# Kernel optimization log

Hardware: AMD Instinct MI355X
Metric: run time of the kernel (lower is better)

The kernel has to match this reference:

```python
import jax, jax.numpy as jnp
import numpy as np

C, H, W = 32, 64, 64
KH, KW = 5, 5
OH, OW = 60, 60
N_IN = C * H * W
B, S = 64, 4096
CAP = 128


def _build_indices():
    # Enumerate every (c, kh, kw, oh, ow) slot of the unfold, matching
    # fold(unfold(order)) in the torch module (stride 1, pad 0, dilation 1).
    c = np.arange(C)[:, None, None, None, None]
    kh = np.arange(KH)[None, :, None, None, None]
    kw = np.arange(KW)[None, None, :, None, None]
    oh = np.arange(OH)[None, None, None, :, None]
    ow = np.arange(OW)[None, None, None, None, :]
    ids = c * (H * W) + (oh + kh) * W + (ow + kw)          # input flat id feeding slot
    ckk = c * (KH * KW) + kh * KW + kw                     # kernel-local channel index
    j = ckk * (OH * OW) + oh * OW + ow                     # flat slot in order_convoled
    ids, j = np.broadcast_arrays(ids, j)
    ids = ids.ravel().astype(np.int64)
    j = j.ravel().astype(np.int64)
    perm = np.argsort(ids, kind='stable')
    sid, sj = ids[perm], j[perm]
    counts = np.bincount(ids, minlength=N_IN)
    Lmax = int(counts.max())                               # = 25 here
    starts = np.concatenate([[0], np.cumsum(counts)[:-1]])
    rank = np.arange(sid.shape[0]) - starts[sid]
    indices = np.full((N_IN, Lmax), -1, dtype=np.int32)
    indices[sid, rank] = sj
    return indices


def setup_inputs() -> dict:
    key = jax.random.key(0)
    spikes = jax.random.randint(key, (B, S, 1, 1), 0, N_IN, dtype=jnp.int32)
    indices = jnp.asarray(_build_indices())
    return {"spikes": spikes, "indices": indices, "out_h": OH, "out_w": OW, "cap": CAP}


def reference(spikes, indices, out_h, out_w, cap):
    Bn, Sn = spikes.shape[0], spikes.shape[1]
    L = indices.shape[1]
    nbins = out_h * out_w
    E = Sn * L                                             # events per batch element

    ids = spikes[:, :, 0, 0]                               # [B,S] flat input ids
    g = indices[ids]                                       # [B,S,L] slots, -1 padded
    valid = g >= 0
    j = jnp.where(valid, g, 0)
    bins = (j % nbins).reshape(Bn * E)                     # output bin (oh*out_w+ow)
    ckk = (j // nbins).reshape(Bn * E)                     # kernel-local index to store
    valid_f = valid.reshape(Bn * E)
    b_idx = jnp.repeat(jnp.arange(Bn, dtype=jnp.int32), E)

    # Arrival-order rank within each (batch, bin): stable sort by global bin,
    # then rank = position - segment start (running max of change points).
    gbin = jnp.where(valid_f, b_idx * nbins + bins, Bn * nbins)   # sentinel for invalid
    perm = jnp.argsort(gbin)                               # stable
    sorted_gbin = gbin[perm]
    pos = jnp.arange(Bn * E, dtype=jnp.int32)
    change = jnp.concatenate([jnp.ones((1,), bool), sorted_gbin[1:] != sorted_gbin[:-1]])
    seg_start = jax.lax.cummax(jnp.where(change, pos, 0))
    rank_sorted = pos - seg_start
    rank = jnp.zeros(Bn * E, jnp.int32).at[perm].set(rank_sorted)  # inverse perm

    # Scatter ckk into per-bin slots; invalid / overflow events go to slot=cap (dropped).
    slot = jnp.where(valid_f & (rank < cap), rank, cap)
    out = jnp.full((Bn, cap + 1, nbins), -1, dtype=spikes.dtype)
    out = out.at[b_idx, slot, bins].set(jnp.where(valid_f, ckk, -1), mode='drop')
    return out[:, :cap].reshape(Bn, cap, out_h, out_w)
```

## Files before the change

kernel.cpp:

```cpp
#include <hip/hip_runtime.h>

#define OHh   60
#define OWw   60
#define NBINS (OHh * OWw)
#define NB    64
#define NS    4096
#define CAP   128

#define NW     4
#define SEG    (NS / NW)
#define CH     (SEG / 64)
#define HCAP   160
#define PRE0   64

__global__ __launch_bounds__(256) void sort_spikes_row4(
    const int* __restrict__ spikes, int* __restrict__ out) {
    const int bid  = (int)blockIdx.x;
    const int b    = bid & (NB - 1);
    const int row  = bid >> 6;
    const int tid  = (int)threadIdx.x;
    const int wv   = tid >> 6;
    const int lane = tid & 63;
    const bool valid = lane < OWw;

    __shared__ int            hitbuf[NW][256];
    __shared__ unsigned       pres[NW][64][7];
    __shared__ unsigned short outimg[PRE0][OWw];
    __shared__ int            cnt[NW][64];
    __shared__ int            ovf;

    if (tid == 0) ovf = 0;
#pragma unroll
    for (int i = 0; i < 5; ++i) pres[wv][lane][i] = 0u;

    {
        int* oi = (int*)&outimg[0][0];
        for (int i = tid; i < PRE0 * OWw / 2; i += 256) oi[i] = -1;
    }

    const int* __restrict__ sp   = spikes + b * NS + wv * SEG;
    int* __restrict__       outb = out + (size_t)b * (CAP * NBINS) + row * OWw;

    int vs[CH];
#pragma unroll
    for (int c = 0; c < CH; ++c) vs[c] = sp[c * 64 + lane];

    int* const hb_w = &hitbuf[wv][0];
    const int row5 = row * 5;

    int hbase = 0;
#pragma unroll
    for (int c = 0; c < CH; ++c) {
        const int v = vs[c];
        const int h = (v >> 6) & 63;
        const int w = v & 63;
        const int A = (v >> 12) * 25 + h * 5 + w - row5;
        const int R = (w << 16) | A;
        const bool halo = (unsigned)(h - row) < 5u;

        const unsigned long long mask = __ballot(halo);
        const int pos = __builtin_amdgcn_mbcnt_hi(
            (unsigned)(mask >> 32),
            __builtin_amdgcn_mbcnt_lo((unsigned)mask, 0));
        if (halo) hb_w[min(hbase + pos, 255)] = R;
        hbase += (int)__popcll(mask);

        if (valid) outb[(PRE0 + wv * CH + c) * NBINS + lane] = -1;
    }
    if (hbase > HCAP && lane == 0) ovf = 1;
    const int n = min(hbase, HCAP);

    const int qi  = (lane < OWw) ? (lane / 5) : 4096;
    const int kwc = lane - qi * 5;
    for (int hbi = 0; hbi < n; hbi += 12) {
        const int hidx = hbi + qi;
        const int R    = hb_w[min(hidx, 255)];
        const int bin  = (R >> 16) - kwc;
        if (((unsigned)bin < 60u) && (hidx < n)) {
            atomicOr(&pres[wv][bin][hidx >> 5], 1u << (hidx & 31));
        }
    }

    unsigned m0 = pres[wv][lane][0], m1 = pres[wv][lane][1];
    unsigned m2 = pres[wv][lane][2], m3 = pres[wv][lane][3];
    unsigned m4 = pres[wv][lane][4];
    cnt[wv][lane] = __builtin_popcount(m0) + __builtin_popcount(m1) +
                    __builtin_popcount(m2) + __builtin_popcount(m3) +
                    __builtin_popcount(m4);
    __syncthreads();

    if (ovf == 0) {
        if (valid) {
            int k = 0;
            for (int w = 0; w < wv; ++w) k += cnt[w][lane];
            unsigned mw[5] = {m0, m1, m2, m3, m4};
#pragma unroll
            for (int wd = 0; wd < 5; ++wd) {
                unsigned mm = mw[wd];
                while (mm) {
                    const int j = __builtin_ctz(mm);
                    mm &= mm - 1;
                    const int src = wd * 32 + j;
                    const int ck  = (hb_w[src] & 0xffff) - lane;
                    if (k < PRE0) outimg[k][lane] = (unsigned short)ck;
                    else if (k < CAP) outb[k * NBINS + lane] = ck;
                    ++k;
                }
            }
        }
        __syncthreads();
        if (valid) {
#pragma unroll 4
            for (int i = 0; i < PRE0 / NW; ++i) {
                const int kk = wv * (PRE0 / NW) + i;
                outb[kk * NBINS + lane] = (int)(short)outimg[kk][lane];
            }
        }
    } else if (wv == 0) {
        const int* __restrict__ spf = spikes + b * NS;
        int cc = 0;
        for (int c = 0; c < NS / 64; ++c) {
            const int v = spf[c * 64 + lane];
            const int h = (v >> 6) & 63;
            unsigned long long mask = __ballot((unsigned)(h - row) < 5u);
            while (mask) {
                const int j = (int)__builtin_ctzll(mask);
                mask &= mask - 1;
                const int vj =
                    __builtin_amdgcn_readlane(v, __builtin_amdgcn_readfirstlane(j));
                const int wj  = vj & 63;
                const int khj = ((vj >> 6) & 63) - row;
                const int cj  = vj >> 12;
                const int kw  = wj - lane;
                if (((unsigned)kw < 5u) & valid) {
                    if (cc < CAP)
                        outb[cc * NBINS + lane] = cj * 25 + khj * 5 + kw;
                    ++cc;
                }
            }
        }
        if (valid)
            for (int k = cc; k < CAP; ++k) outb[k * NBINS + lane] = -1;
    }
}

extern "C" void kernel_launch(void* const* d_in, const int* in_sizes, int n_in,
                              void* d_out, int out_size, void* d_ws, size_t ws_size,
                              hipStream_t stream) {
    const int* spikes = (const int*)d_in[0];
    int* out = (int*)d_out;

    dim3 grid(OHh * NB);
    dim3 block(256);
    sort_spikes_row4<<<grid, block, 0, stream>>>(spikes, out);
}
```

Baseline: 138.4 us.

## Process two output rows per block to share spike loading and halo filtering

New measurement: 145.9 us. 5.4% more time.

```diff
diff --git a/kernel.cpp b/kernel.cpp
--- a/kernel.cpp
+++ b/kernel.cpp
@@ -8,64 +8,76 @@
 #define CAP   128
 
 #define NW     4
+#define RPB    2
+#define RG     (OHh / RPB)
 #define SEG    (NS / NW)
 #define CH     (SEG / 64)
 #define HCAP   160
+#define HBUF   176
+#define PW     5
 #define PRE0   64
 
-__global__ __launch_bounds__(256) void sort_spikes_row4(
+__global__ __launch_bounds__(256) void sort_spikes_pair(
     const int* __restrict__ spikes, int* __restrict__ out) {
     const int bid  = (int)blockIdx.x;
     const int b    = bid & (NB - 1);
-    const int row  = bid >> 6;
+    const int rg   = bid >> 6;
     const int tid  = (int)threadIdx.x;
     const int wv   = tid >> 6;
     const int lane = tid & 63;
     const bool valid = lane < OWw;
+    const int row0 = rg * RPB;
 
-    __shared__ int            hitbuf[NW][256];
-    __shared__ unsigned       pres[NW][64][7];
+    __shared__ int            hitbuf[NW][HBUF];
+    __shared__ unsigned       pres[NW][RPB][64][PW];
     __shared__ unsigned short outimg[PRE0][OWw];
-    __shared__ int            cnt[NW][64];
+    __shared__ int            cnt[NW][RPB][64];
     __shared__ int            ovf;
 
     if (tid == 0) ovf = 0;
 #pragma unroll
-    for (int i = 0; i < 5; ++i) pres[wv][lane][i] = 0u;
-
+    for (int i = 0; i < PW; ++i) {
+        pres[wv][0][lane][i] = 0u;
+        pres[wv][1][lane][i] = 0u;
+    }
     {
         int* oi = (int*)&outimg[0][0];
         for (int i = tid; i < PRE0 * OWw / 2; i += 256) oi[i] = -1;
     }
 
-    const int* __restrict__ sp   = spikes + b * NS + wv * SEG;
-    int* __restrict__       outb = out + (size_t)b * (CAP * NBINS) + row * OWw;
+    const int* __restrict__ sp = spikes + b * NS + wv * SEG;
+    int* __restrict__ outb0 = out + (size_t)b * (CAP * NBINS) + row0 * OWw;
+    int* __restrict__ outb1 = outb0 + OWw;
 
     int vs[CH];
 #pragma unroll
     for (int c = 0; c < CH; ++c) vs[c] = sp[c * 64 + lane];
 
     int* const hb_w = &hitbuf[wv][0];
-    const int row5 = row * 5;
 
     int hbase = 0;
 #pragma unroll
     for (int c = 0; c < CH; ++c) {
-        const int v = vs[c];
-        const int h = (v >> 6) & 63;
-        const int w = v & 63;
-        const int A = (v >> 12) * 25 + h * 5 + w - row5;
-        const int R = (w << 16) | A;
-        const bool halo = (unsigned)(h - row) < 5u;
+        const int v   = vs[c];
+        const int h   = (v >> 6) & 63;
+        const int kh6 = h - row0;
+        const bool halo = (unsigned)kh6 < 6u;
+        const int w   = v & 63;
+        const int A   = (v >> 12) * 25 + kh6 * 5 + w;
+        const int R   = (kh6 << 16) | (w << 10) | A;
 
         const unsigned long long mask = __ballot(halo);
         const int pos = __builtin_amdgcn_mbcnt_hi(
             (unsigned)(mask >> 32),
             __builtin_amdgcn_mbcnt_lo((unsigned)mask, 0));
-        if (halo) hb_w[min(hbase + pos, 255)] = R;
+        if (halo) hb_w[min(hbase + pos, HBUF - 1)] = R;
         hbase += (int)__popcll(mask);
 
-        if (valid) outb[(PRE0 + wv * CH + c) * NBINS + lane] = -1;
+        if (valid) {
+            const int so = (PRE0 + wv * CH + c) * NBINS + lane;
+            outb0[so] = -1;
+            outb1[so] = -1;
+        }
     }
     if (hbase > HCAP && lane == 0) ovf = 1;
     const int n = min(hbase, HCAP);
@@ -74,73 +86,93 @@
     const int kwc = lane - qi * 5;
     for (int hbi = 0; hbi < n; hbi += 12) {
         const int hidx = hbi + qi;
-        const int R    = hb_w[min(hidx, 255)];
-        const int bin  = (R >> 16) - kwc;
-        if (((unsigned)bin < 60u) && (hidx < n)) {
-            atomicOr(&pres[wv][bin][hidx >> 5], 1u << (hidx & 31));
-        }
+        const int R    = hb_w[min(hidx, HBUF - 1)];
+        const int w    = (R >> 10) & 63;
+        const int kh6  = R >> 16;
+        const int bin  = w - kwc;
+        const bool vb  = ((unsigned)bin < 60u) & (hidx < n);
+        const unsigned bit = 1u << (hidx & 31);
+        const int word = hidx >> 5;
+        if (vb & ((unsigned)kh6 < 5u))
+            atomicOr(&pres[wv][0][bin][word], bit);
+        if (vb & ((unsigned)(kh6 - 1) < 5u))
+            atomicOr(&pres[wv][1][bin][word], bit);
     }
 
-    unsigned m0 = pres[wv][lane][0], m1 = pres[wv][lane][1];
-    unsigned m2 = pres[wv][lane][2], m3 = pres[wv][lane][3];
-    unsigned m4 = pres[wv][lane][4];
-    cnt[wv][lane] = __builtin_popcount(m0) + __builtin_popcount(m1) +
-                    __builtin_popcount(m2) + __builtin_popcount(m3) +
-                    __builtin_popcount(m4);
+    unsigned mw[RPB][PW];
+#pragma unroll
+    for (int j = 0; j < RPB; ++j) {
+        unsigned s = 0;
+#pragma unroll
+        for (int i = 0; i < PW; ++i) {
+            mw[j][i] = pres[wv][j][lane][i];
+            s += __builtin_popcount(mw[j][i]);
+        }
+        cnt[wv][j][lane] = (int)s;
+    }
     __syncthreads();
 
     if (ovf == 0) {
-        if (valid) {
-            int k = 0;
-            for (int w = 0; w < wv; ++w) k += cnt[w][lane];
-            unsigned mw[5] = {m0, m1, m2, m3, m4};
 #pragma unroll
-            for (int wd = 0; wd < 5; ++wd) {
-                unsigned mm = mw[wd];
-                while (mm) {
-                    const int j = __builtin_ctz(mm);
-                    mm &= mm - 1;
-                    const int src = wd * 32 + j;
-                    const int ck  = (hb_w[src] & 0xffff) - lane;
-                    if (k < PRE0) outimg[k][lane] = (unsigned short)ck;
-                    else if (k < CAP) outb[k * NBINS + lane] = ck;
-                    ++k;
+        for (int j = 0; j < RPB; ++j) {
+            int* __restrict__ outbj = (j == 0) ? outb0 : outb1;
+            if (valid) {
+                int k = 0;
+                for (int wq = 0; wq < wv; ++wq) k += cnt[wq][j][lane];
+                const int sub = lane + 5 * j;
+#pragma unroll
+                for (int wd = 0; wd < PW; ++wd) {
+                    unsigned mm = mw[j][wd];
+                    while (mm) {
+                        const int t = __builtin_ctz(mm);
+                        mm &= mm - 1;
+                        const int src = wd * 32 + t;
+                        const int ck  = (hb_w[src] & 0x3ff) - sub;
+                        if (k < PRE0) outimg[k][lane] = (unsigned short)ck;
+                        else if (k < CAP) outbj[k * NBINS + lane] = ck;
+                        ++k;
+                    }
                 }
             }
+            __syncthreads();
+            if (valid) {
+#pragma unroll 4
+                for (int i = 0; i < PRE0 / NW; ++i) {
+                    const int kk  = wv * (PRE0 / NW) + i;
+                    const int val = (int)(short)outimg[kk][lane];
+                    if (j == 0) outimg[kk][lane] = 0xFFFFu;
+                    outbj[kk * NBINS + lane] = val;
+                }
+            }
+            if (j == 0) __syncthreads();
         }
-        __syncthreads();
-        if (valid) {
-#pragma unroll 4
-            for (int i = 0; i < PRE0 / NW; ++i) {
-                const int kk = wv * (PRE0 / NW) + i;
-                outb[kk * NBINS + lane] = (int)(short)outimg[kk][lane];
-            }
-        }
-    } else if (wv == 0) {
+    } else if (wv < RPB) {
+        const int rowf = row0 + wv;
+        int* __restrict__ outbf = (wv == 0) ? outb0 : outb1;
         const int* __restrict__ spf = spikes + b * NS;
         int cc = 0;
         for (int c = 0; c < NS / 64; ++c) {
             const int v = spf[c * 64 + lane];
             const int h = (v >> 6) & 63;
-            unsigned long long mask = __ballot((unsigned)(h - row) < 5u);
+            unsigned long long mask = __ballot((unsigned)(h - rowf) < 5u);
             while (mask) {
                 const int j = (int)__builtin_ctzll(mask);
                 mask &= mask - 1;
                 const int vj =
                     __builtin_amdgcn_readlane(v, __builtin_amdgcn_readfirstlane(j));
                 const int wj  = vj & 63;
-                const int khj = ((vj >> 6) & 63) - row;
+                const int khj = ((vj >> 6) & 63) - rowf;
                 const int cj  = vj >> 12;
                 const int kw  = wj - lane;
                 if (((unsigned)kw < 5u) & valid) {
                     if (cc < CAP)
-                        outb[cc * NBINS + lane] = cj * 25 + khj * 5 + kw;
+                        outbf[cc * NBINS + lane] = cj * 25 + khj * 5 + kw;
                     ++cc;
                 }
             }
         }
         if (valid)
-            for (int k = cc; k < CAP; ++k) outb[k * NBINS + lane] = -1;
+            for (int k = cc; k < CAP; ++k) outbf[k * NBINS + lane] = -1;
     }
 }
 
@@ -150,7 +182,7 @@
     const int* spikes = (const int*)d_in[0];
     int* out = (int*)d_out;
 
-    dim3 grid(OHh * NB);
+    dim3 grid(RG * NB);
     dim3 block(256);
-    sort_spikes_row4<<<grid, block, 0, stream>>>(spikes, out);
+    sort_spikes_pair<<<grid, block, 0, stream>>>(spikes, out);
 }
```
